# Kernel tuning notes

Measured on AMD Instinct MI355X. Metric: run time of the kernel, lower is better.

## Reference

```python
import jax, jax.numpy as jnp
import numpy as np
import math

B, S, D, H = 2, 2048, 1024, 16
DK = D // H

def setup_inputs() -> dict:
    key = jax.random.key(0)
    ks = jax.random.split(key, 12)
    s = 1.0 / math.sqrt(D)
    inp = {
        'input_q': jax.random.normal(ks[0], (B, S, D), jnp.float32),
        'input_k': jax.random.normal(ks[1], (B, S, D), jnp.float32),
        'input_v': jax.random.normal(ks[2], (B, S, D), jnp.float32),
        'mask': jax.random.randint(ks[3], (B, 1, S, S), 0, 2, jnp.int32),
        'Wq': jax.random.normal(ks[4], (D, D), jnp.float32) * s,
        'bq': jnp.zeros((D,), jnp.float32),
        'Wk': jax.random.normal(ks[5], (D, D), jnp.float32) * s,
        'bk': jnp.zeros((D,), jnp.float32),
        'Wv': jax.random.normal(ks[6], (D, D), jnp.float32) * s,
        'bv': jnp.zeros((D,), jnp.float32),
        'Wo': jax.random.normal(ks[7], (D, D), jnp.float32) * s,
        'bo': jnp.zeros((D,), jnp.float32),
    }
    return inp

def reference(input_q, input_k, input_v, mask, Wq, bq, Wk, bk, Wv, bv, Wo, bo):
    # Linear projections (torch Linear: x @ W.T + b), split into heads: [B,H,S,DK]
    q = (input_q @ Wq.T + bq).reshape(B, S, H, DK).transpose(0, 2, 1, 3)
    k = (input_k @ Wk.T + bk).reshape(B, S, H, DK).transpose(0, 2, 1, 3)
    v = (input_v @ Wv.T + bv).reshape(B, S, H, DK).transpose(0, 2, 1, 3)
    scores = jnp.einsum('bhqd,bhkd->bhqk', q, k) / math.sqrt(DK)
    scores = jnp.where(mask == 0, jnp.float32(-1e9), scores)
    attn = jax.nn.softmax(scores, axis=-1)
    out = jnp.einsum('bhqk,bhkd->bhqd', attn, v)
    out = out.transpose(0, 2, 1, 3).reshape(B, S, D)
    return out @ Wo.T + bo
```

## Files before the change

kernel.cpp:

```cpp
#include <hip/hip_runtime.h>
#include <math.h>

#define kB 2
#define kS 2048
#define kD 1024
#define kH 16
#define kM (kB * kS)

#define kC 0.180336880f

typedef unsigned short u16;
typedef unsigned int u32;
typedef unsigned long long u64;
typedef short s16x8 __attribute__((ext_vector_type(8)));
typedef float f32x4 __attribute__((ext_vector_type(4)));

#if __has_builtin(__builtin_amdgcn_exp2f)
#define EXP2(x) __builtin_amdgcn_exp2f(x)
#else
#define EXP2(x) exp2f(x)
#endif

__device__ __forceinline__ u16 f2bf(float f) {
    u32 u = __float_as_uint(f);
    u += 0x7FFFu + ((u >> 16) & 1u);
    return (u16)(u >> 16);
}

__device__ __forceinline__ u32 cvt_pk_bf16(float lo, float hi) {
    u32 r;
    asm("v_cvt_pk_bf16_f32 %0, %1, %2" : "=v"(r) : "v"(lo), "v"(hi));
    return r;
}

typedef __attribute__((address_space(1))) void as1_void;
typedef __attribute__((address_space(3))) void as3_void;
__device__ __forceinline__ void async_copy16(const void* g, void* l) {
    __builtin_amdgcn_global_load_lds((as1_void*)(unsigned long long)g,
                                     (as3_void*)(unsigned)(unsigned long long)l,
                                     16, 0, 0);
}

__global__ __launch_bounds__(256) void prep(
        const float* __restrict__ xq, const float* __restrict__ xk, const float* __restrict__ xv,
        const float* __restrict__ Wq, const float* __restrict__ Wk,
        const float* __restrict__ Wv, const float* __restrict__ Wo,
        const int* __restrict__ msk,
        u16* __restrict__ xqb, u16* __restrict__ xkb, u16* __restrict__ xvb,
        u16* __restrict__ wqb, u16* __restrict__ wkb, u16* __restrict__ wvb,
        u16* __restrict__ wob, u64* __restrict__ prepM) {
    const int bid = blockIdx.x;
    const int tid = threadIdx.x;
    if (bid < 16384) {
        const float* in;
        u16* out;
        int i;
        float sc = 1.0f;
        if (bid < 12288) {
            const int z = bid >> 12;
            in = z == 0 ? xq : (z == 1 ? xk : xv);
            out = z == 0 ? xqb : (z == 1 ? xkb : xvb);
            i = (bid & 4095) * 256 + tid;
        } else {
            const int z = (bid - 12288) >> 10;
            in = z == 0 ? Wq : (z == 1 ? Wk : (z == 2 ? Wv : Wo));
            out = z == 0 ? wqb : (z == 1 ? wkb : (z == 2 ? wvb : wob));
            if (z == 0) sc = kC;
            i = ((bid - 12288) & 1023) * 256 + tid;
        }
        const float4 v = ((const float4*)in)[i];
        ushort4 o;
        o.x = f2bf(v.x * sc); o.y = f2bf(v.y * sc);
        o.z = f2bf(v.z * sc); o.w = f2bf(v.w * sc);
        ((ushort4*)out)[i] = o;
    } else {
        const int wid = (bid - 16384) * 4 + (tid >> 6);
        const int lane = tid & 63;
        const int kt = wid & 31, qb = (wid >> 5) & 127, b = wid >> 12;
        const int q = qb * 16 + (lane & 15);
        const int kbase = kt * 64 + ((lane >> 4) << 2);
        const int* mrow = msk + ((size_t)b * kS + q) * kS;
        u64 keep = 0;
#pragma unroll
        for (int c = 0; c < 4; ++c) {
            const int4 m4 = *(const int4*)(mrow + kbase + c * 16);
            const int mv[4] = {m4.x, m4.y, m4.z, m4.w};
#pragma unroll
            for (int r = 0; r < 4; ++r) {
                const u64 bl = __ballot(mv[r] != 0);
                if (lane == c * 4 + r) keep = bl;
            }
        }
        if (lane < 16)
            prepM[(((size_t)b * 128 + qb) * 32 + kt) * 16 + lane] = keep;
    }
}

template <int MODE, int TILEM, int TILEN>
__device__ __forceinline__ void gemm_bt_body(const u16* __restrict__ A,
                                             const u16* __restrict__ W,
                                             const float* __restrict__ bias,
                                             void* __restrict__ Cp,
                                             const float bscale,
                                             u16* __restrict__ AsM,
                                             u16* __restrict__ BsM,
                                             const int bxi, const int byi) {
    constexpr int FM = TILEM / 32;
    constexpr int FN = TILEN / 32;
    u16* As0 = AsM;            u16* As1 = AsM + TILEM * 32;
    u16* Bs0 = BsM;            u16* Bs1 = BsM + TILEN * 32;
    const int tid = threadIdx.x;
    const int wave = tid >> 6, lane = tid & 63;
    const int l15 = lane & 15, quad = lane >> 4;
    const int wr = wave >> 1, wc = wave & 1;
    const int m0 = (MODE == 3 ? bxi : byi) * TILEM;
    const int n0 = (MODE == 3 ? byi : bxi) * TILEN;

    const int srow = lane >> 2;
    const int schk = ((lane & 3) - ((lane >> 3) & 3)) & 3;
    const u16* gA = A + (size_t)(m0 + (TILEM / 4) * wave + srow) * kD + schk * 8;
    const u16* gB = W + (size_t)(n0 + (TILEN / 4) * wave + srow) * kD + schk * 8;

    f32x4 acc[FM][FN];
#pragma unroll
    for (int i = 0; i < FM; ++i)
#pragma unroll
        for (int j = 0; j < FN; ++j) acc[i][j] = (f32x4)0.f;

    auto STAGE = [&](int kt, u16* dA, u16* dB) {
#pragma unroll
        for (int i = 0; i < TILEM / 64; ++i)
            async_copy16(gA + (size_t)(16 * i) * kD + kt,
                         dA + (wave * (TILEM / 64) + i) * 512);
#pragma unroll
        for (int i = 0; i < TILEN / 64; ++i)
            async_copy16(gB + (size_t)(16 * i) * kD + kt,
                         dB + (wave * (TILEN / 64) + i) * 512);
    };

    const int ro = ((quad + (l15 >> 1)) & 3) * 8;
    auto COMPUTE = [&](const u16* sA, const u16* sB) {
        s16x8 af[FM], bf[FN];
#pragma unroll
        for (int fm = 0; fm < FM; ++fm)
            af[fm] = *(const s16x8*)(sA + (wr * (TILEM / 32) + fm) * 512 + l15 * 32 + ro);
#pragma unroll
        for (int fn = 0; fn < FN; ++fn)
            bf[fn] = *(const s16x8*)(sB + (wc * (TILEN / 32) + fn) * 512 + l15 * 32 + ro);
#pragma unroll
        for (int fm = 0; fm < FM; ++fm)
#pragma unroll
            for (int fn = 0; fn < FN; ++fn)
                acc[fm][fn] = __builtin_amdgcn_mfma_f32_16x16x32_bf16(
                    af[fm], bf[fn], acc[fm][fn], 0, 0, 0);
    };

    STAGE(0, As0, Bs0);
    __syncthreads();
    for (int kt = 0; kt < kD; kt += 64) {
        if (kt + 32 < kD) STAGE(kt + 32, As1, Bs1);
        COMPUTE(As0, Bs0);
        __syncthreads();
        if (kt + 64 < kD) STAGE(kt + 64, As0, Bs0);
        COMPUTE(As1, Bs1);
        __syncthreads();
    }

    if constexpr (MODE == 3) {
#pragma unroll
        for (int fn = 0; fn < FN; ++fn) {
            const int sglob = n0 + wc * (TILEN / 2) + fn * 16 + l15;
            const int bb = sglob >> 11, ss = sglob & (kS - 1);
#pragma unroll
            for (int fm = 0; fm < FM; ++fm) {
                const int dglob = m0 + wr * (TILEM / 2) + fm * 16 + quad * 4;
                const float4 b4 = *(const float4*)(bias + dglob);
                const float bb4[4] = {b4.x * bscale, b4.y * bscale,
                                      b4.z * bscale, b4.w * bscale};
                const int hh = dglob >> 6, dd = dglob & 63;
                u16* base = (u16*)Cp + ((size_t)(bb * kH + hh) * 64 + dd) * kS + ss;
#pragma unroll
                for (int r = 0; r < 4; ++r)
                    base[(size_t)r * kS] = f2bf(acc[fm][fn][r] + bb4[r]);
            }
        }
    } else {
#pragma unroll
        for (int fn = 0; fn < FN; ++fn) {
            const int col = n0 + wc * (TILEN / 2) + fn * 16 + l15;
            const float bv = bias[col] * bscale;
#pragma unroll
            for (int fm = 0; fm < FM; ++fm) {
                const int row = m0 + wr * (TILEM / 2) + fm * 16 + quad * 4;
#pragma unroll
                for (int r = 0; r < 4; ++r) {
                    const float v = acc[fm][fn][r] + bv;
                    if constexpr (MODE == 0)
                        ((u16*)Cp)[(size_t)(row + r) * kD + col] = f2bf(v);
                    else
                        ((float*)Cp)[(size_t)(row + r) * kD + col] = v;
                }
            }
        }
    }
}

__global__ __launch_bounds__(256) void qkv_gemm(
        const u16* __restrict__ xq, const u16* __restrict__ xk, const u16* __restrict__ xv,
        const u16* __restrict__ wq, const u16* __restrict__ wk, const u16* __restrict__ wv,
        const float* __restrict__ bq, const float* __restrict__ bk, const float* __restrict__ bv,
        u16* __restrict__ q, u16* __restrict__ k, u16* __restrict__ vt) {
    __shared__ u16 AsM[2 * 128 * 32];
    __shared__ u16 BsM[2 * 64 * 32];
    const int id = blockIdx.y * 16 + blockIdx.x;
    const int g = id & 7, mm = id >> 3;
    const int z = blockIdx.z;
    if (z == 2) {
        const int bm = mm >> 3;
        const int bn = g * 8 + (mm & 7);
        gemm_bt_body<3, 128, 64>(wv, xv, bv, vt, 1.f, AsM, BsM, bm, bn);
    } else {
        const int by = g * 4 + (mm & 3);
        const int bx = mm >> 2;
        if (z == 0) gemm_bt_body<0, 128, 64>(xq, wq, bq, q, kC, AsM, BsM, bx, by);
        else        gemm_bt_body<0, 128, 64>(xk, wk, bk, k, 1.f, AsM, BsM, bx, by);
    }
}

__global__ __launch_bounds__(256) void o_gemm(const u16* __restrict__ A,
                                              const u16* __restrict__ W,
                                              const float* __restrict__ bias,
                                              float* __restrict__ C) {
    __shared__ u16 AsM[2 * 64 * 32];
    __shared__ u16 BsM[2 * 64 * 32];
    const int id = blockIdx.y * 16 + blockIdx.x;
    const int g = id & 7, mm = id >> 3;
    const int by = g * 8 + (mm & 7);
    const int bx = mm >> 3;
    gemm_bt_body<2, 64, 64>(A, W, bias, C, 1.f, AsM, BsM, bx, by);
}

__device__ __forceinline__ void attn_tile(
        const int kt, u16* __restrict__ cur, u16* __restrict__ nxt, const bool do_stage,
        const u16* __restrict__ gK0, const u16* __restrict__ gV0,
        const u64* __restrict__ mbase,
        const s16x8 bq0, const s16x8 bq1, const s16x8 onesf,
        u16* __restrict__ psrow,
        f32x4 oacc[4], f32x4& lacc,
        const int l15, const int quad, const int l7, const int wave) {
    if (do_stage) {
        async_copy16(gK0 + (size_t)(kt + 64) * kD, nxt + (8 * wave) * 64);
        async_copy16(gV0 + kt + 64, nxt + 4096 + (8 * wave) * 64);
    }
    const u64* mt = mbase + (kt >> 6) * 16;
    u64 mk[16];
#pragma unroll
    for (int i = 0; i < 16; ++i) mk[i] = mt[i];

    f32x4 s[4];
#pragma unroll
    for (int fn = 0; fn < 4; ++fn) s[fn] = (f32x4)0.f;
    __builtin_amdgcn_s_setprio(1);
#pragma unroll
    for (int kc = 0; kc < 2; ++kc) {
        const s16x8 bqf = kc ? bq1 : bq0;
#pragma unroll
        for (int fn = 0; fn < 4; ++fn) {
            const s16x8 ak = *(const s16x8*)(cur + (fn * 16 + l15) * 64 + ((kc * 4 + quad) ^ l7) * 8);
            s[fn] = __builtin_amdgcn_mfma_f32_16x16x32_bf16(ak, bqf, s[fn], 0, 0, 0);
        }
    }
    __builtin_amdgcn_s_setprio(0);

    s16x8 av[2][4];
#pragma unroll
    for (int kc = 0; kc < 2; ++kc)
#pragma unroll
        for (int fd = 0; fd < 4; ++fd)
            av[kc][fd] = *(const s16x8*)(cur + 4096 + (fd * 16 + l15) * 64 + ((kc * 4 + quad) ^ l7) * 8);

#pragma unroll
    for (int fn = 0; fn < 4; ++fn)
#pragma unroll
        for (int r = 0; r < 4; ++r) {
            const float p = EXP2(s[fn][r]);
            float pm;
            asm("v_cndmask_b32 %0, 0, %1, %2" : "=v"(pm) : "v"(p), "s"(mk[fn * 4 + r]));
            s[fn][r] = pm;
        }

#pragma unroll
    for (int fn = 0; fn < 4; ++fn) {
        uint2 o;
        o.x = cvt_pk_bf16(s[fn][0], s[fn][1]);
        o.y = cvt_pk_bf16(s[fn][2], s[fn][3]);
        const int chunk = fn * 2 + (quad >> 1);
        *(uint2*)(psrow + ((chunk ^ l7) * 8) + (quad & 1) * 4) = o;
    }

    __builtin_amdgcn_s_setprio(1);
#pragma unroll
    for (int kc = 0; kc < 2; ++kc) {
        const s16x8 bp = *(const s16x8*)(psrow + ((kc * 4 + quad) ^ l7) * 8);
        lacc = __builtin_amdgcn_mfma_f32_16x16x32_bf16(onesf, bp, lacc, 0, 0, 0);
#pragma unroll
        for (int fd = 0; fd < 4; ++fd)
            oacc[fd] = __builtin_amdgcn_mfma_f32_16x16x32_bf16(av[kc][fd], bp, oacc[fd], 0, 0, 0);
    }
    __builtin_amdgcn_s_setprio(0);
    __syncthreads();
}

__global__ __launch_bounds__(512) void attn_mfma(const u16* __restrict__ Qb,
                                                 const u16* __restrict__ Kb,
                                                 const u16* __restrict__ Vt,
                                                 const u64* __restrict__ prepM,
                                                 u16* __restrict__ Ob) {
    __shared__ u16 Bs2[2][8192];
    __shared__ u16 Ps[8192];

    const int tid = threadIdx.x;
    const int wave = tid >> 6, lane = tid & 63;
    const int l15 = lane & 15, quad = lane >> 4, l7 = lane & 7;
    const int q0 = blockIdx.x * 128;
    const int b = blockIdx.y >> 4, h = blockIdx.y & 15;

    const int srow = lane >> 3;
    const int schk = l7 ^ srow;

    {
        const u16* g0 = Qb + ((size_t)(b * kS + q0 + 16 * wave + srow)) * kD + h * 64 + schk * 8;
        async_copy16(g0, Ps + (16 * wave) * 64);
        async_copy16(g0 + 8 * kD, Ps + (16 * wave + 8) * 64);
    }
    const u16* gK0 = Kb + ((size_t)(b * kS + 8 * wave + srow)) * kD + h * 64 + schk * 8;
    const u16* gV0 = Vt + ((size_t)((b * kH + h) * 64 + 8 * wave + srow)) * kS + schk * 8;
    async_copy16(gK0, Bs2[0] + (8 * wave) * 64);
    async_copy16(gV0, Bs2[0] + 4096 + (8 * wave) * 64);

    const int wave_u = __builtin_amdgcn_readfirstlane(wave);
    const u64* mbase = prepM + (((size_t)b * 128 + blockIdx.x * 8 + wave_u) * 32) * 16;

    s16x8 onesf;
#pragma unroll
    for (int i = 0; i < 8; ++i) onesf[i] = (short)0x3F80;

    f32x4 oacc[4];
#pragma unroll
    for (int i = 0; i < 4; ++i) oacc[i] = (f32x4)0.f;
    f32x4 lacc = (f32x4)0.f;

    __syncthreads();
    s16x8 bq0, bq1;
    bq0 = *(const s16x8*)(Ps + (16 * wave + l15) * 64 + ((0 + quad) ^ l7) * 8);
    bq1 = *(const s16x8*)(Ps + (16 * wave + l15) * 64 + ((4 + quad) ^ l7) * 8);
    u16* psrow = Ps + (16 * wave + l15) * 64;

    for (int ti = 0; ti < 32; ti += 2) {
        attn_tile(ti * 64, Bs2[0], Bs2[1], true,
                  gK0, gV0, mbase, bq0, bq1, onesf, psrow, oacc, lacc,
                  l15, quad, l7, wave);
        attn_tile(ti * 64 + 64, Bs2[1], Bs2[0], ti + 2 < 32,
                  gK0, gV0, mbase, bq0, bq1, onesf, psrow, oacc, lacc,
                  l15, quad, l7, wave);
    }

    const float inv = 1.f / lacc[0];
    const size_t orow = (size_t)(b * kS + q0 + 16 * wave + l15);
#pragma unroll
    for (int fd = 0; fd < 4; ++fd) {
        uint2 o;
        o.x = cvt_pk_bf16(oacc[fd][0] * inv, oacc[fd][1] * inv);
        o.y = cvt_pk_bf16(oacc[fd][2] * inv, oacc[fd][3] * inv);
        *(uint2*)(Ob + orow * kD + h * 64 + fd * 16 + quad * 4) = o;
    }
}

extern "C" void kernel_launch(void* const* d_in, const int* in_sizes, int n_in,
                              void* d_out, int out_size, void* d_ws, size_t ws_size,
                              hipStream_t stream) {
    const float* xq = (const float*)d_in[0];
    const float* xk = (const float*)d_in[1];
    const float* xv = (const float*)d_in[2];
    const int*  msk = (const int*)d_in[3];
    const float* Wq = (const float*)d_in[4];
    const float* bq = (const float*)d_in[5];
    const float* Wk = (const float*)d_in[6];
    const float* bk = (const float*)d_in[7];
    const float* Wv = (const float*)d_in[8];
    const float* bv = (const float*)d_in[9];
    const float* Wo = (const float*)d_in[10];
    const float* bo = (const float*)d_in[11];
    float* out = (float*)d_out;

    const size_t NX = (size_t)kM * kD;
    const size_t NW = (size_t)kD * kD;

    u64* prepM = (u64*)d_ws;
    u16* p = (u16*)((char*)d_ws + (1 << 20));
    u16* xqb = p; p += NX;
    u16* xkb = p; p += NX;
    u16* xvb = p; p += NX;
    u16* wqb = p; p += NW;
    u16* wkb = p; p += NW;
    u16* wvb = p; p += NW;
    u16* wob = p; p += NW;
    u16* qb  = p; p += NX;
    u16* kb  = p; p += NX;
    u16* vtb = p; p += NX;
    u16* ab  = xqb;

    prep<<<18432, 256, 0, stream>>>(xq, xk, xv, Wq, Wk, Wv, Wo, msk,
                                    xqb, xkb, xvb, wqb, wkb, wvb, wob, prepM);

    dim3 gq(kD / 64, kM / 128, 3);
    qkv_gemm<<<gq, 256, 0, stream>>>(xqb, xkb, xvb, wqb, wkb, wvb, bq, bk, bv, qb, kb, vtb);

    dim3 ga(kS / 128, kB * kH);
    attn_mfma<<<ga, 512, 0, stream>>>(qb, kb, vtb, prepM, ab);

    dim3 go(kD / 64, kM / 64);
    o_gemm<<<go, 256, 0, stream>>>(ab, wob, bo, out);
}
```

Before: 244.8 us.

## Software-pipeline attention loop: overlap next tile's QK MFMA with current softmax/PV

Restructures the attention inner loop so the QK^T scores for tile t are computed while the exp/mask/PV stage of tile t-1 runs, with a prologue and epilogue to handle the first and last tiles. This lets the exp and LDS round-trip of the probability tile overlap with matrix-core work instead of serializing. It also adds a min-blocks-per-CU hint to launch_bounds, which caps register usage and may cause spills, especially since the pipelined form keeps an extra score tile live.

```diff
diff --git a/kernel.cpp b/kernel.cpp
--- a/kernel.cpp
+++ b/kernel.cpp
@@ -240,82 +240,11 @@
     gemm_bt_body<2, 64, 64>(A, W, bias, C, 1.f, AsM, BsM, bx, by);
 }
 
-__device__ __forceinline__ void attn_tile(
-        const int kt, u16* __restrict__ cur, u16* __restrict__ nxt, const bool do_stage,
-        const u16* __restrict__ gK0, const u16* __restrict__ gV0,
-        const u64* __restrict__ mbase,
-        const s16x8 bq0, const s16x8 bq1, const s16x8 onesf,
-        u16* __restrict__ psrow,
-        f32x4 oacc[4], f32x4& lacc,
-        const int l15, const int quad, const int l7, const int wave) {
-    if (do_stage) {
-        async_copy16(gK0 + (size_t)(kt + 64) * kD, nxt + (8 * wave) * 64);
-        async_copy16(gV0 + kt + 64, nxt + 4096 + (8 * wave) * 64);
-    }
-    const u64* mt = mbase + (kt >> 6) * 16;
-    u64 mk[16];
-#pragma unroll
-    for (int i = 0; i < 16; ++i) mk[i] = mt[i];
-
-    f32x4 s[4];
-#pragma unroll
-    for (int fn = 0; fn < 4; ++fn) s[fn] = (f32x4)0.f;
-    __builtin_amdgcn_s_setprio(1);
-#pragma unroll
-    for (int kc = 0; kc < 2; ++kc) {
-        const s16x8 bqf = kc ? bq1 : bq0;
-#pragma unroll
-        for (int fn = 0; fn < 4; ++fn) {
-            const s16x8 ak = *(const s16x8*)(cur + (fn * 16 + l15) * 64 + ((kc * 4 + quad) ^ l7) * 8);
-            s[fn] = __builtin_amdgcn_mfma_f32_16x16x32_bf16(ak, bqf, s[fn], 0, 0, 0);
-        }
-    }
-    __builtin_amdgcn_s_setprio(0);
-
-    s16x8 av[2][4];
-#pragma unroll
-    for (int kc = 0; kc < 2; ++kc)
-#pragma unroll
-        for (int fd = 0; fd < 4; ++fd)
-            av[kc][fd] = *(const s16x8*)(cur + 4096 + (fd * 16 + l15) * 64 + ((kc * 4 + quad) ^ l7) * 8);
-
-#pragma unroll
-    for (int fn = 0; fn < 4; ++fn)
-#pragma unroll
-        for (int r = 0; r < 4; ++r) {
-            const float p = EXP2(s[fn][r]);
-            float pm;
-            asm("v_cndmask_b32 %0, 0, %1, %2" : "=v"(pm) : "v"(p), "s"(mk[fn * 4 + r]));
-            s[fn][r] = pm;
-        }
-
-#pragma unroll
-    for (int fn = 0; fn < 4; ++fn) {
-        uint2 o;
-        o.x = cvt_pk_bf16(s[fn][0], s[fn][1]);
-        o.y = cvt_pk_bf16(s[fn][2], s[fn][3]);
-        const int chunk = fn * 2 + (quad >> 1);
-        *(uint2*)(psrow + ((chunk ^ l7) * 8) + (quad & 1) * 4) = o;
-    }
-
-    __builtin_amdgcn_s_setprio(1);
-#pragma unroll
-    for (int kc = 0; kc < 2; ++kc) {
-        const s16x8 bp = *(const s16x8*)(psrow + ((kc * 4 + quad) ^ l7) * 8);
-        lacc = __builtin_amdgcn_mfma_f32_16x16x32_bf16(onesf, bp, lacc, 0, 0, 0);
-#pragma unroll
-        for (int fd = 0; fd < 4; ++fd)
-            oacc[fd] = __builtin_amdgcn_mfma_f32_16x16x32_bf16(av[kc][fd], bp, oacc[fd], 0, 0, 0);
-    }
-    __builtin_amdgcn_s_setprio(0);
-    __syncthreads();
-}
-
-__global__ __launch_bounds__(512) void attn_mfma(const u16* __restrict__ Qb,
-                                                 const u16* __restrict__ Kb,
-                                                 const u16* __restrict__ Vt,
-                                                 const u64* __restrict__ prepM,
-                                                 u16* __restrict__ Ob) {
+__global__ __launch_bounds__(512, 4) void attn_mfma(const u16* __restrict__ Qb,
+                                                    const u16* __restrict__ Kb,
+                                                    const u16* __restrict__ Vt,
+                                                    const u64* __restrict__ prepM,
+                                                    u16* __restrict__ Ob) {
     __shared__ u16 Bs2[2][8192];
     __shared__ u16 Ps[8192];
 
@@ -356,13 +285,94 @@
     bq1 = *(const s16x8*)(Ps + (16 * wave + l15) * 64 + ((4 + quad) ^ l7) * 8);
     u16* psrow = Ps + (16 * wave + l15) * 64;
 
-    for (int ti = 0; ti < 32; ti += 2) {
-        attn_tile(ti * 64, Bs2[0], Bs2[1], true,
-                  gK0, gV0, mbase, bq0, bq1, onesf, psrow, oacc, lacc,
-                  l15, quad, l7, wave);
-        attn_tile(ti * 64 + 64, Bs2[1], Bs2[0], ti + 2 < 32,
-                  gK0, gV0, mbase, bq0, bq1, onesf, psrow, oacc, lacc,
-                  l15, quad, l7, wave);
+    f32x4 sp[4];
+    s16x8 av[2][4];
+
+    auto QK = [&](const u16* cur, f32x4 sc[4]) {
+#pragma unroll
+        for (int fn = 0; fn < 4; ++fn) sc[fn] = (f32x4)0.f;
+        __builtin_amdgcn_s_setprio(1);
+#pragma unroll
+        for (int kc = 0; kc < 2; ++kc) {
+            const s16x8 bqf = kc ? bq1 : bq0;
+#pragma unroll
+            for (int fn = 0; fn < 4; ++fn) {
+                const s16x8 ak = *(const s16x8*)(cur + (fn * 16 + l15) * 64 + ((kc * 4 + quad) ^ l7) * 8);
+                sc[fn] = __builtin_amdgcn_mfma_f32_16x16x32_bf16(ak, bqf, sc[fn], 0, 0, 0);
+            }
+        }
+        __builtin_amdgcn_s_setprio(0);
+    };
+    auto SMPV = [&](const u64* mk) {
+#pragma unroll
+        for (int fn = 0; fn < 4; ++fn)
+#pragma unroll
+            for (int r = 0; r < 4; ++r) {
+                const float p = EXP2(sp[fn][r]);
+                float pm;
+                asm("v_cndmask_b32 %0, 0, %1, %2" : "=v"(pm) : "v"(p), "s"(mk[fn * 4 + r]));
+                sp[fn][r] = pm;
+            }
+#pragma unroll
+        for (int fn = 0; fn < 4; ++fn) {
+            uint2 o;
+            o.x = cvt_pk_bf16(sp[fn][0], sp[fn][1]);
+            o.y = cvt_pk_bf16(sp[fn][2], sp[fn][3]);
+            const int chunk = fn * 2 + (quad >> 1);
+            *(uint2*)(psrow + ((chunk ^ l7) * 8) + (quad & 1) * 4) = o;
+        }
+        __builtin_amdgcn_s_setprio(1);
+#pragma unroll
+        for (int kc = 0; kc < 2; ++kc) {
+            const s16x8 bp = *(const s16x8*)(psrow + ((kc * 4 + quad) ^ l7) * 8);
+            lacc = __builtin_amdgcn_mfma_f32_16x16x32_bf16(onesf, bp, lacc, 0, 0, 0);
+#pragma unroll
+            for (int fd = 0; fd < 4; ++fd)
+                oacc[fd] = __builtin_amdgcn_mfma_f32_16x16x32_bf16(av[kc][fd], bp, oacc[fd], 0, 0, 0);
+        }
+        __builtin_amdgcn_s_setprio(0);
+    };
+    auto AV = [&](const u16* cur) {
+#pragma unroll
+        for (int kc = 0; kc < 2; ++kc)
+#pragma unroll
+            for (int fd = 0; fd < 4; ++fd)
+                av[kc][fd] = *(const s16x8*)(cur + 4096 + (fd * 16 + l15) * 64 + ((kc * 4 + quad) ^ l7) * 8);
+    };
+
+    async_copy16(gK0 + (size_t)64 * kD, Bs2[1] + (8 * wave) * 64);
+    async_copy16(gV0 + 64, Bs2[1] + 4096 + (8 * wave) * 64);
+    QK(Bs2[0], sp);
+    AV(Bs2[0]);
+    __syncthreads();
+
+    for (int t = 1; t < 32; ++t) {
+        u16* cur = Bs2[t & 1];
+        u16* nxt = Bs2[(t + 1) & 1];
+        if (t < 31) {
+            async_copy16(gK0 + (size_t)((t + 1) * 64) * kD, nxt + (8 * wave) * 64);
+            async_copy16(gV0 + (t + 1) * 64, nxt + 4096 + (8 * wave) * 64);
+        }
+        const u64* mt = mbase + (t - 1) * 16;
+        u64 mk[16];
+#pragma unroll
+        for (int i = 0; i < 16; ++i) mk[i] = mt[i];
+
+        f32x4 sc[4];
+        QK(cur, sc);
+        SMPV(mk);
+        AV(cur);
+#pragma unroll
+        for (int fn = 0; fn < 4; ++fn) sp[fn] = sc[fn];
+        __syncthreads();
+    }
+
+    {
+        const u64* mt = mbase + 31 * 16;
+        u64 mk[16];
+#pragma unroll
+        for (int i = 0; i < 16; ++i) mk[i] = mt[i];
+        SMPV(mk);
     }
 
     const float inv = 1.f / lacc[0];
```

New measurement: 246.7 us. No clear change (+0.8%).

## Double attention key tile to 128 to halve barriers per pass

Applied to the files above, without the earlier changes.

Raises the K/V tile processed per pipeline step from 64 to 128 keys, so there are 16 iterations instead of 32 and half as many __syncthreads. Each wave now stages two K rows and two V chunks per step, and the P->V stage is split into two 64-key halves that reuse the P scratch row. Shared memory for the double buffer doubles (to 64 KB plus P), which may lower occupancy, and the larger score array raises register pressure.

```diff
diff --git a/kernel.cpp b/kernel.cpp
--- a/kernel.cpp
+++ b/kernel.cpp
@@ -241,7 +241,7 @@
 }
 
 __device__ __forceinline__ void attn_tile(
-        const int kt, u16* __restrict__ cur, u16* __restrict__ nxt, const bool do_stage,
+        const int t, u16* __restrict__ cur, u16* __restrict__ nxt, const bool do_stage,
         const u16* __restrict__ gK0, const u16* __restrict__ gV0,
         const u64* __restrict__ mbase,
         const s16x8 bq0, const s16x8 bq1, const s16x8 onesf,
@@ -249,65 +249,65 @@
         f32x4 oacc[4], f32x4& lacc,
         const int l15, const int quad, const int l7, const int wave) {
     if (do_stage) {
-        async_copy16(gK0 + (size_t)(kt + 64) * kD, nxt + (8 * wave) * 64);
-        async_copy16(gV0 + kt + 64, nxt + 4096 + (8 * wave) * 64);
-    }
-    const u64* mt = mbase + (kt >> 6) * 16;
-    u64 mk[16];
-#pragma unroll
-    for (int i = 0; i < 16; ++i) mk[i] = mt[i];
-
-    f32x4 s[4];
-#pragma unroll
-    for (int fn = 0; fn < 4; ++fn) s[fn] = (f32x4)0.f;
+        const int kn = (t + 1) * 128;
+        async_copy16(gK0 + (size_t)kn * kD, nxt + (16 * wave) * 64);
+        async_copy16(gK0 + (size_t)(kn + 8) * kD, nxt + (16 * wave + 8) * 64);
+        async_copy16(gV0 + kn, nxt + 8192 + (8 * wave) * 64);
+        async_copy16(gV0 + kn + 64, nxt + 12288 + (8 * wave) * 64);
+    }
+    const u64* mt = mbase + (size_t)t * 32;
+
+    f32x4 s[8];
+#pragma unroll
+    for (int fn = 0; fn < 8; ++fn) s[fn] = (f32x4)0.f;
     __builtin_amdgcn_s_setprio(1);
 #pragma unroll
     for (int kc = 0; kc < 2; ++kc) {
         const s16x8 bqf = kc ? bq1 : bq0;
 #pragma unroll
-        for (int fn = 0; fn < 4; ++fn) {
+        for (int fn = 0; fn < 8; ++fn) {
             const s16x8 ak = *(const s16x8*)(cur + (fn * 16 + l15) * 64 + ((kc * 4 + quad) ^ l7) * 8);
             s[fn] = __builtin_amdgcn_mfma_f32_16x16x32_bf16(ak, bqf, s[fn], 0, 0, 0);
         }
     }
     __builtin_amdgcn_s_setprio(0);
 
-    s16x8 av[2][4];
-#pragma unroll
-    for (int kc = 0; kc < 2; ++kc)
-#pragma unroll
-        for (int fd = 0; fd < 4; ++fd)
-            av[kc][fd] = *(const s16x8*)(cur + 4096 + (fd * 16 + l15) * 64 + ((kc * 4 + quad) ^ l7) * 8);
-
-#pragma unroll
-    for (int fn = 0; fn < 4; ++fn)
-#pragma unroll
-        for (int r = 0; r < 4; ++r) {
-            const float p = EXP2(s[fn][r]);
-            float pm;
-            asm("v_cndmask_b32 %0, 0, %1, %2" : "=v"(pm) : "v"(p), "s"(mk[fn * 4 + r]));
-            s[fn][r] = pm;
-        }
-
-#pragma unroll
-    for (int fn = 0; fn < 4; ++fn) {
-        uint2 o;
-        o.x = cvt_pk_bf16(s[fn][0], s[fn][1]);
-        o.y = cvt_pk_bf16(s[fn][2], s[fn][3]);
-        const int chunk = fn * 2 + (quad >> 1);
-        *(uint2*)(psrow + ((chunk ^ l7) * 8) + (quad & 1) * 4) = o;
-    }
-
-    __builtin_amdgcn_s_setprio(1);
-#pragma unroll
-    for (int kc = 0; kc < 2; ++kc) {
-        const s16x8 bp = *(const s16x8*)(psrow + ((kc * 4 + quad) ^ l7) * 8);
-        lacc = __builtin_amdgcn_mfma_f32_16x16x32_bf16(onesf, bp, lacc, 0, 0, 0);
-#pragma unroll
-        for (int fd = 0; fd < 4; ++fd)
-            oacc[fd] = __builtin_amdgcn_mfma_f32_16x16x32_bf16(av[kc][fd], bp, oacc[fd], 0, 0, 0);
-    }
-    __builtin_amdgcn_s_setprio(0);
+#pragma unroll
+    for (int h = 0; h < 2; ++h) {
+        u64 mk[16];
+#pragma unroll
+        for (int i = 0; i < 16; ++i) mk[i] = mt[h * 16 + i];
+#pragma unroll
+        for (int f2 = 0; f2 < 4; ++f2)
+#pragma unroll
+            for (int r = 0; r < 4; ++r) {
+                const float p = EXP2(s[h * 4 + f2][r]);
+                float pm;
+                asm("v_cndmask_b32 %0, 0, %1, %2" : "=v"(pm) : "v"(p), "s"(mk[f2 * 4 + r]));
+                s[h * 4 + f2][r] = pm;
+            }
+#pragma unroll
+        for (int f2 = 0; f2 < 4; ++f2) {
+            uint2 o;
+            o.x = cvt_pk_bf16(s[h * 4 + f2][0], s[h * 4 + f2][1]);
+            o.y = cvt_pk_bf16(s[h * 4 + f2][2], s[h * 4 + f2][3]);
+            const int chunk = f2 * 2 + (quad >> 1);
+            *(uint2*)(psrow + ((chunk ^ l7) * 8) + (quad & 1) * 4) = o;
+        }
+        const u16* Vh = cur + 8192 + h * 4096;
+        __builtin_amdgcn_s_setprio(1);
+#pragma unroll
+        for (int kc = 0; kc < 2; ++kc) {
+            const s16x8 bp = *(const s16x8*)(psrow + ((kc * 4 + quad) ^ l7) * 8);
+            lacc = __builtin_amdgcn_mfma_f32_16x16x32_bf16(onesf, bp, lacc, 0, 0, 0);
+#pragma unroll
+            for (int fd = 0; fd < 4; ++fd) {
+                const s16x8 av = *(const s16x8*)(Vh + (fd * 16 + l15) * 64 + ((kc * 4 + quad) ^ l7) * 8);
+                oacc[fd] = __builtin_amdgcn_mfma_f32_16x16x32_bf16(av, bp, oacc[fd], 0, 0, 0);
+            }
+        }
+        __builtin_amdgcn_s_setprio(0);
+    }
     __syncthreads();
 }
 
@@ -316,7 +316,7 @@
                                                  const u16* __restrict__ Vt,
                                                  const u64* __restrict__ prepM,
                                                  u16* __restrict__ Ob) {
-    __shared__ u16 Bs2[2][8192];
+    __shared__ u16 Bs2[2][16384];
     __shared__ u16 Ps[8192];
 
     const int tid = threadIdx.x;
@@ -333,10 +333,12 @@
         async_copy16(g0, Ps + (16 * wave) * 64);
         async_copy16(g0 + 8 * kD, Ps + (16 * wave + 8) * 64);
     }
-    const u16* gK0 = Kb + ((size_t)(b * kS + 8 * wave + srow)) * kD + h * 64 + schk * 8;
+    const u16* gK0 = Kb + ((size_t)(b * kS + 16 * wave + srow)) * kD + h * 64 + schk * 8;
     const u16* gV0 = Vt + ((size_t)((b * kH + h) * 64 + 8 * wave + srow)) * kS + schk * 8;
-    async_copy16(gK0, Bs2[0] + (8 * wave) * 64);
-    async_copy16(gV0, Bs2[0] + 4096 + (8 * wave) * 64);
+    async_copy16(gK0, Bs2[0] + (16 * wave) * 64);
+    async_copy16(gK0 + (size_t)8 * kD, Bs2[0] + (16 * wave + 8) * 64);
+    async_copy16(gV0, Bs2[0] + 8192 + (8 * wave) * 64);
+    async_copy16(gV0 + 64, Bs2[0] + 12288 + (8 * wave) * 64);
 
     const int wave_u = __builtin_amdgcn_readfirstlane(wave);
     const u64* mbase = prepM + (((size_t)b * 128 + blockIdx.x * 8 + wave_u) * 32) * 16;
@@ -356,11 +358,11 @@
     bq1 = *(const s16x8*)(Ps + (16 * wave + l15) * 64 + ((4 + quad) ^ l7) * 8);
     u16* psrow = Ps + (16 * wave + l15) * 64;
 
-    for (int ti = 0; ti < 32; ti += 2) {
-        attn_tile(ti * 64, Bs2[0], Bs2[1], true,
+    for (int ti = 0; ti < 16; ti += 2) {
+        attn_tile(ti, Bs2[0], Bs2[1], true,
                   gK0, gV0, mbase, bq0, bq1, onesf, psrow, oacc, lacc,
                   l15, quad, l7, wave);
-        attn_tile(ti * 64 + 64, Bs2[1], Bs2[0], ti + 2 < 32,
+        attn_tile(ti + 1, Bs2[1], Bs2[0], ti + 2 < 16,
                   gK0, gV0, mbase, bq0, bq1, onesf, psrow, oacc, lacc,
                   l15, quad, l7, wave);
     }
```

Measured after the change: 244.4 us. Within noise of the previous version (-0.2%).

## Fuse fp32-to-bf16 activation conversion into QKV GEMM tile loads

Applied to the files above, without the earlier changes.

Drops the separate conversion pass that turned the three fp32 activation tensors into bf16 buffers. The QKV GEMM now loads fp32 activation tiles into registers, packs them to bf16 and writes them to LDS itself, while weights still use async global-to-LDS copies. This removes one full write and read of the bf16 activation copies and shrinks the prep grid. In exchange the GEMM reads twice the bytes per activation tile, and the register staging (load before compute, write after) may give weaker latency hiding than the async LDS copy path.

```diff
diff --git a/kernel.cpp b/kernel.cpp
--- a/kernel.cpp
+++ b/kernel.cpp
@@ -42,39 +42,26 @@
 }
 
 __global__ __launch_bounds__(256) void prep(
-        const float* __restrict__ xq, const float* __restrict__ xk, const float* __restrict__ xv,
         const float* __restrict__ Wq, const float* __restrict__ Wk,
         const float* __restrict__ Wv, const float* __restrict__ Wo,
         const int* __restrict__ msk,
-        u16* __restrict__ xqb, u16* __restrict__ xkb, u16* __restrict__ xvb,
         u16* __restrict__ wqb, u16* __restrict__ wkb, u16* __restrict__ wvb,
         u16* __restrict__ wob, u64* __restrict__ prepM) {
     const int bid = blockIdx.x;
     const int tid = threadIdx.x;
-    if (bid < 16384) {
-        const float* in;
-        u16* out;
-        int i;
-        float sc = 1.0f;
-        if (bid < 12288) {
-            const int z = bid >> 12;
-            in = z == 0 ? xq : (z == 1 ? xk : xv);
-            out = z == 0 ? xqb : (z == 1 ? xkb : xvb);
-            i = (bid & 4095) * 256 + tid;
-        } else {
-            const int z = (bid - 12288) >> 10;
-            in = z == 0 ? Wq : (z == 1 ? Wk : (z == 2 ? Wv : Wo));
-            out = z == 0 ? wqb : (z == 1 ? wkb : (z == 2 ? wvb : wob));
-            if (z == 0) sc = kC;
-            i = ((bid - 12288) & 1023) * 256 + tid;
-        }
+    if (bid < 4096) {
+        const int z = bid >> 10;
+        const float* in = z == 0 ? Wq : (z == 1 ? Wk : (z == 2 ? Wv : Wo));
+        u16* out = z == 0 ? wqb : (z == 1 ? wkb : (z == 2 ? wvb : wob));
+        const float sc = (z == 0) ? kC : 1.0f;
+        const int i = (bid & 1023) * 256 + tid;
         const float4 v = ((const float4*)in)[i];
         ushort4 o;
         o.x = f2bf(v.x * sc); o.y = f2bf(v.y * sc);
         o.z = f2bf(v.z * sc); o.w = f2bf(v.w * sc);
         ((ushort4*)out)[i] = o;
     } else {
-        const int wid = (bid - 16384) * 4 + (tid >> 6);
+        const int wid = (bid - 4096) * 4 + (tid >> 6);
         const int lane = tid & 63;
         const int kt = wid & 31, qb = (wid >> 5) & 127, b = wid >> 12;
         const int q = qb * 16 + (lane & 15);
@@ -96,9 +83,9 @@
     }
 }
 
-template <int MODE, int TILEM, int TILEN>
-__device__ __forceinline__ void gemm_bt_body(const u16* __restrict__ A,
-                                             const u16* __restrict__ W,
+template <int MODE, int TILEM, int TILEN, int CVT>
+__device__ __forceinline__ void gemm_bt_body(const void* __restrict__ Aop,
+                                             const void* __restrict__ Bop,
                                              const float* __restrict__ bias,
                                              void* __restrict__ Cp,
                                              const float bscale,
@@ -118,8 +105,15 @@
 
     const int srow = lane >> 2;
     const int schk = ((lane & 3) - ((lane >> 3) & 3)) & 3;
-    const u16* gA = A + (size_t)(m0 + (TILEM / 4) * wave + srow) * kD + schk * 8;
-    const u16* gB = W + (size_t)(n0 + (TILEN / 4) * wave + srow) * kD + schk * 8;
+    const u16* gA16 = (const u16*)Aop + (size_t)(m0 + (TILEM / 4) * wave + srow) * kD + schk * 8;
+    const u16* gB16 = (const u16*)Bop + (size_t)(n0 + (TILEN / 4) * wave + srow) * kD + schk * 8;
+
+    const int arow = lane >> 1, ah = lane & 1;
+    const float* gAf = (const float*)Aop + (size_t)(m0 + 32 * wave + arow) * kD + ah * 16;
+    const int brow = lane >> 2, bc = lane & 3;
+    const float* gBf = (const float*)Bop + (size_t)(n0 + 16 * wave + brow) * kD + bc * 8;
+
+    float4 rf[4];
 
     f32x4 acc[FM][FN];
 #pragma unroll
@@ -127,15 +121,55 @@
 #pragma unroll
         for (int j = 0; j < FN; ++j) acc[i][j] = (f32x4)0.f;
 
-    auto STAGE = [&](int kt, u16* dA, u16* dB) {
-#pragma unroll
-        for (int i = 0; i < TILEM / 64; ++i)
-            async_copy16(gA + (size_t)(16 * i) * kD + kt,
-                         dA + (wave * (TILEM / 64) + i) * 512);
-#pragma unroll
-        for (int i = 0; i < TILEN / 64; ++i)
-            async_copy16(gB + (size_t)(16 * i) * kD + kt,
-                         dB + (wave * (TILEN / 64) + i) * 512);
+    auto STAGE_LOAD = [&](int kt, u16* dA, u16* dB) {
+        if constexpr (CVT == 1) {
+#pragma unroll
+            for (int i = 0; i < 4; ++i) rf[i] = *(const float4*)(gAf + kt + i * 4);
+        }
+        if constexpr (CVT == 2) {
+#pragma unroll
+            for (int i = 0; i < 2; ++i) rf[i] = *(const float4*)(gBf + kt + i * 4);
+        }
+        if constexpr (CVT != 1) {
+#pragma unroll
+            for (int i = 0; i < TILEM / 64; ++i)
+                async_copy16(gA16 + (size_t)(16 * i) * kD + kt,
+                             dA + (wave * (TILEM / 64) + i) * 512);
+        }
+        if constexpr (CVT != 2) {
+#pragma unroll
+            for (int i = 0; i < TILEN / 64; ++i)
+                async_copy16(gB16 + (size_t)(16 * i) * kD + kt,
+                             dB + (wave * (TILEN / 64) + i) * 512);
+        }
+    };
+
+    auto STAGE_WRITE = [&](u16* dA, u16* dB) {
+        if constexpr (CVT == 1) {
+            const int r16 = arow & 15;
+            u16* base = dA + (wave * 2 + (arow >> 4)) * 512 + r16 * 32;
+            const int rot = r16 >> 1;
+            uint4 w;
+            w.x = cvt_pk_bf16(rf[0].x, rf[0].y);
+            w.y = cvt_pk_bf16(rf[0].z, rf[0].w);
+            w.z = cvt_pk_bf16(rf[1].x, rf[1].y);
+            w.w = cvt_pk_bf16(rf[1].z, rf[1].w);
+            *(uint4*)(base + ((2 * ah + rot) & 3) * 8) = w;
+            w.x = cvt_pk_bf16(rf[2].x, rf[2].y);
+            w.y = cvt_pk_bf16(rf[2].z, rf[2].w);
+            w.z = cvt_pk_bf16(rf[3].x, rf[3].y);
+            w.w = cvt_pk_bf16(rf[3].z, rf[3].w);
+            *(uint4*)(base + ((2 * ah + 1 + rot) & 3) * 8) = w;
+        }
+        if constexpr (CVT == 2) {
+            u16* base = dB + wave * 512 + brow * 32;
+            uint4 w;
+            w.x = cvt_pk_bf16(rf[0].x, rf[0].y);
+            w.y = cvt_pk_bf16(rf[0].z, rf[0].w);
+            w.z = cvt_pk_bf16(rf[1].x, rf[1].y);
+            w.w = cvt_pk_bf16(rf[1].z, rf[1].w);
+            *(uint4*)(base + ((bc + (brow >> 1)) & 3) * 8) = w;
+        }
     };
 
     const int ro = ((quad + (l15 >> 1)) & 3) * 8;
@@ -155,14 +189,17 @@
                     af[fm], bf[fn], acc[fm][fn], 0, 0, 0);
     };
 
-    STAGE(0, As0, Bs0);
+    STAGE_LOAD(0, As0, Bs0);
+    STAGE_WRITE(As0, Bs0);
     __syncthreads();
     for (int kt = 0; kt < kD; kt += 64) {
-        if (kt + 32 < kD) STAGE(kt + 32, As1, Bs1);
+        if (kt + 32 < kD) STAGE_LOAD(kt + 32, As1, Bs1);
         COMPUTE(As0, Bs0);
+        if (kt + 32 < kD) STAGE_WRITE(As1, Bs1);
         __syncthreads();
-        if (kt + 64 < kD) STAGE(kt + 64, As0, Bs0);
+        if (kt + 64 < kD) STAGE_LOAD(kt + 64, As0, Bs0);
         COMPUTE(As1, Bs1);
+        if (kt + 64 < kD) STAGE_WRITE(As0, Bs0);
         __syncthreads();
     }
 
@@ -206,7 +243,7 @@
 }
 
 __global__ __launch_bounds__(256) void qkv_gemm(
-        const u16* __restrict__ xq, const u16* __restrict__ xk, const u16* __restrict__ xv,
+        const float* __restrict__ xq, const float* __restrict__ xk, const float* __restrict__ xv,
         const u16* __restrict__ wq, const u16* __restrict__ wk, const u16* __restrict__ wv,
         const float* __restrict__ bq, const float* __restrict__ bk, const float* __restrict__ bv,
         u16* __restrict__ q, u16* __restrict__ k, u16* __restrict__ vt) {
@@ -218,12 +255,12 @@
     if (z == 2) {
         const int bm = mm >> 3;
         const int bn = g * 8 + (mm & 7);
-        gemm_bt_body<3, 128, 64>(wv, xv, bv, vt, 1.f, AsM, BsM, bm, bn);
+        gemm_bt_body<3, 128, 64, 2>(wv, xv, bv, vt, 1.f, AsM, BsM, bm, bn);
     } else {
         const int by = g * 4 + (mm & 3);
         const int bx = mm >> 2;
-        if (z == 0) gemm_bt_body<0, 128, 64>(xq, wq, bq, q, kC, AsM, BsM, bx, by);
-        else        gemm_bt_body<0, 128, 64>(xk, wk, bk, k, 1.f, AsM, BsM, bx, by);
+        if (z == 0) gemm_bt_body<0, 128, 64, 1>(xq, wq, bq, q, kC, AsM, BsM, bx, by);
+        else        gemm_bt_body<0, 128, 64, 1>(xk, wk, bk, k, 1.f, AsM, BsM, bx, by);
     }
 }
 
@@ -237,7 +274,7 @@
     const int g = id & 7, mm = id >> 3;
     const int by = g * 8 + (mm & 7);
     const int bx = mm >> 3;
-    gemm_bt_body<2, 64, 64>(A, W, bias, C, 1.f, AsM, BsM, bx, by);
+    gemm_bt_body<2, 64, 64, 0>(A, W, bias, C, 1.f, AsM, BsM, bx, by);
 }
 
 __device__ __forceinline__ void attn_tile(
@@ -398,9 +435,7 @@
 
     u64* prepM = (u64*)d_ws;
     u16* p = (u16*)((char*)d_ws + (1 << 20));
-    u16* xqb = p; p += NX;
-    u16* xkb = p; p += NX;
-    u16* xvb = p; p += NX;
+    u16* ab  = p; p += NX;
     u16* wqb = p; p += NW;
     u16* wkb = p; p += NW;
     u16* wvb = p; p += NW;
@@ -408,13 +443,12 @@
     u16* qb  = p; p += NX;
     u16* kb  = p; p += NX;
     u16* vtb = p; p += NX;
-    u16* ab  = xqb;
-
-    prep<<<18432, 256, 0, stream>>>(xq, xk, xv, Wq, Wk, Wv, Wo, msk,
-                                    xqb, xkb, xvb, wqb, wkb, wvb, wob, prepM);
+
+    prep<<<6144, 256, 0, stream>>>(Wq, Wk, Wv, Wo, msk,
+                                   wqb, wkb, wvb, wob, prepM);
 
     dim3 gq(kD / 64, kM / 128, 3);
-    qkv_gemm<<<gq, 256, 0, stream>>>(xqb, xkb, xvb, wqb, wkb, wvb, bq, bk, bv, qb, kb, vtb);
+    qkv_gemm<<<gq, 256, 0, stream>>>(xq, xk, xv, wqb, wkb, wvb, bq, bk, bv, qb, kb, vtb);
 
     dim3 ga(kS / 128, kB * kH);
     attn_mfma<<<ga, 512, 0, stream>>>(qb, kb, vtb, prepM, ab);
```

Measured after the change: 274.4 us. +12.1%, slower.
